# Kernel optimization log

Measured on AMD Instinct MI355X. Metric: run time of the kernel, lower is better.

Reference implementation:

```python
import jax, jax.numpy as jnp
import numpy as np

B, S, F, D, M = 2, 512, 16384, 768, 262144  # batch, seq, n_features, d_model, n_connections


def setup_inputs() -> dict:
    key = jax.random.key(0)
    k1, k2, k3, k4, k5 = jax.random.split(key, 5)
    up_facts = jax.random.normal(k1, (B, S, F), dtype=jnp.float32)
    down_encoder = jax.random.normal(k2, (F, D), dtype=jnp.float32) * 0.02
    up_decoder = jax.random.normal(k3, (D, F), dtype=jnp.float32) * 0.02
    i_indices = jnp.sort(jax.random.randint(k4, (M,), 0, F, dtype=jnp.int32)).astype(jnp.int64)
    j_indices = jax.random.randint(k5, (M,), 0, F, dtype=jnp.int32).astype(jnp.int64)
    return {
        "up_facts": up_facts,
        "down_encoder": down_encoder,
        "up_decoder": up_decoder,
        "i_indices": i_indices,
        "j_indices": j_indices,
    }


def reference(up_facts, down_encoder, up_decoder, i_indices, j_indices):
    # Virtual weight value for each sparse connection (i -> j):
    #   values[m] = <down_encoder[i_m, :], up_decoder[:, j_m]>
    values = jnp.sum(down_encoder[i_indices] * up_decoder[:, j_indices].T, axis=1)  # [M]
    # Gather upstream feature activations for each connection, scale by value.
    scaled = up_facts[:, :, j_indices] * values  # [B, S, M]
    # Scatter-add into downstream feature slots (duplicate i indices accumulate).
    contributions = jnp.zeros((up_facts.shape[0], up_facts.shape[1], down_encoder.shape[0]),
                              dtype=up_facts.dtype)
    return contributions.at[:, :, i_indices].add(scaled)  # [B, S, F]
```

## Files before the change

### kernel.cpp

```cpp
#include <hip/hip_runtime.h>
#include <hip/hip_bf16.h>

#define D_DIM 768
#define F_DIM 16384
#define M_CONN 262144
#define N_ROWS 1024

typedef float f32x4 __attribute__((ext_vector_type(4)));
typedef unsigned short u16x4 __attribute__((ext_vector_type(4)));

__device__ __forceinline__ float bf2f(unsigned short u) {
    return __uint_as_float(((unsigned int)u) << 16);
}

__global__ __launch_bounds__(512, 4) void transpose_f2b_t(const float* __restrict__ in,
                                                          unsigned short* __restrict__ out,
                                                          int R, int C) {
    __shared__ unsigned short ldsT[128][260];
    const int t = threadIdx.x;
    const int x0 = blockIdx.x * 128;
    const int y0 = blockIdx.y * 256;
    f32x4 v[16];
#pragma unroll
    for (int it = 0; it < 16; ++it) {
        const int idx = it * 512 + t;
        const int r = idx >> 5;
        const int c4 = idx & 31;
        v[it] = __builtin_nontemporal_load(
            (const f32x4*)(in + (size_t)(y0 + r) * C + x0 + c4 * 4));
    }
#pragma unroll
    for (int it = 0; it < 16; ++it) {
        const int idx = it * 512 + t;
        const int r = idx >> 5;
        const int c4 = idx & 31;
        __hip_bfloat16 b0 = __float2bfloat16(v[it].x);
        __hip_bfloat16 b1 = __float2bfloat16(v[it].y);
        __hip_bfloat16 b2 = __float2bfloat16(v[it].z);
        __hip_bfloat16 b3 = __float2bfloat16(v[it].w);
        ldsT[c4 * 4 + 0][r] = *(unsigned short*)&b0;
        ldsT[c4 * 4 + 1][r] = *(unsigned short*)&b1;
        ldsT[c4 * 4 + 2][r] = *(unsigned short*)&b2;
        ldsT[c4 * 4 + 3][r] = *(unsigned short*)&b3;
    }
    __syncthreads();
#pragma unroll
    for (int it = 0; it < 16; ++it) {
        const int idx = it * 512 + t;
        const int c = idx >> 6;
        const int r4 = idx & 63;
        const u16x4 o = *(const u16x4*)&ldsT[c][r4 * 4];
        *(u16x4*)(out + (size_t)(x0 + c) * R + y0 + r4 * 4) = o;
    }
}

__global__ __launch_bounds__(512, 4) void transpose_b2f_t(const unsigned short* __restrict__ in,
                                                          float* __restrict__ out,
                                                          int R, int C) {
    __shared__ unsigned short ldsT[256][130];
    const int t = threadIdx.x;
    const int x0 = blockIdx.x * 256;
    const int y0 = blockIdx.y * 128;
    u16x4 v[16];
#pragma unroll
    for (int it = 0; it < 16; ++it) {
        const int idx = it * 512 + t;
        const int r = idx >> 6;
        const int c4 = idx & 63;
        v[it] = __builtin_nontemporal_load(
            (const u16x4*)(in + (size_t)(y0 + r) * C + x0 + c4 * 4));
    }
#pragma unroll
    for (int it = 0; it < 16; ++it) {
        const int idx = it * 512 + t;
        const int r = idx >> 6;
        const int c4 = idx & 63;
        ldsT[c4 * 4 + 0][r] = v[it].x;
        ldsT[c4 * 4 + 1][r] = v[it].y;
        ldsT[c4 * 4 + 2][r] = v[it].z;
        ldsT[c4 * 4 + 3][r] = v[it].w;
    }
    __syncthreads();
#pragma unroll
    for (int it = 0; it < 16; ++it) {
        const int idx = it * 512 + t;
        const int c = idx >> 5;
        const int r4 = idx & 31;
        const u16x4 o = *(const u16x4*)&ldsT[c][r4 * 4];
        f32x4 f;
        f.x = bf2f(o.x); f.y = bf2f(o.y); f.z = bf2f(o.z); f.w = bf2f(o.w);
        __builtin_nontemporal_store(
            f, (f32x4*)(out + (size_t)(x0 + c) * R + y0 + r4 * 4));
    }
}

__global__ __launch_bounds__(256) void values_kernel(const float* __restrict__ de,
                                                     const unsigned short* __restrict__ udT,
                                                     const int* __restrict__ i_idx,
                                                     const int* __restrict__ j_idx,
                                                     float* __restrict__ values,
                                                     int m0) {
    const int wave = (blockIdx.x * blockDim.x + threadIdx.x) >> 6;
    const int lane = threadIdx.x & 63;
    const int mbase = m0 + wave * 4;

    int ii[4], jj[4];
#pragma unroll
    for (int t = 0; t < 4; ++t) {
        ii[t] = i_idx[mbase + t];
        jj[t] = j_idx[mbase + t];
    }
    ushort4 u[4][3];
#pragma unroll
    for (int t = 0; t < 4; ++t) {
        const ushort4* b = (const ushort4*)(udT + (size_t)jj[t] * D_DIM);
        u[t][0] = b[lane]; u[t][1] = b[lane + 64]; u[t][2] = b[lane + 128];
    }

    int cur_i = -1;
    float4 a0, a1, a2;
#pragma unroll
    for (int t = 0; t < 4; ++t) {
        const int i = ii[t];
        if (i != cur_i) {
            const float4* a = (const float4*)(de + (size_t)i * D_DIM);
            a0 = a[lane]; a1 = a[lane + 64]; a2 = a[lane + 128];
            cur_i = i;
        }
        float s = 0.f;
        s = fmaf(a0.x, bf2f(u[t][0].x), s); s = fmaf(a0.y, bf2f(u[t][0].y), s);
        s = fmaf(a0.z, bf2f(u[t][0].z), s); s = fmaf(a0.w, bf2f(u[t][0].w), s);
        s = fmaf(a1.x, bf2f(u[t][1].x), s); s = fmaf(a1.y, bf2f(u[t][1].y), s);
        s = fmaf(a1.z, bf2f(u[t][1].z), s); s = fmaf(a1.w, bf2f(u[t][1].w), s);
        s = fmaf(a2.x, bf2f(u[t][2].x), s); s = fmaf(a2.y, bf2f(u[t][2].y), s);
        s = fmaf(a2.z, bf2f(u[t][2].z), s); s = fmaf(a2.w, bf2f(u[t][2].w), s);
#pragma unroll
        for (int off = 32; off > 0; off >>= 1)
            s += __shfl_down(s, off, 64);
        if (lane == 0) values[mbase + t] = s;
    }
}

__global__ __launch_bounds__(256) void seg_kernel(const int* __restrict__ i_idx,
                                                  int* __restrict__ seg) {
    const int i = blockIdx.x * blockDim.x + threadIdx.x;
    if (i > F_DIM) return;
    if (i == F_DIM) { seg[i] = M_CONN; return; }
    int lo = 0, hi = M_CONN;
    while (lo < hi) {
        int mid = (lo + hi) >> 1;
        if (i_idx[mid] < i) lo = mid + 1; else hi = mid;
    }
    seg[i] = lo;
}

__global__ __launch_bounds__(256) void spmm_kernel(const unsigned short* __restrict__ upT,
                                                   const int* __restrict__ j_idx,
                                                   const float* __restrict__ vals,
                                                   const int* __restrict__ seg,
                                                   unsigned short* __restrict__ outT,
                                                   int i0) {
    const int i = i0 + blockIdx.x;
    const int t = threadIdx.x;
    const int ms = seg[i], me = seg[i + 1];
    float4 acc0 = make_float4(0.f, 0.f, 0.f, 0.f);
    float4 acc1 = make_float4(0.f, 0.f, 0.f, 0.f);
    float4 acc2 = make_float4(0.f, 0.f, 0.f, 0.f);
    float4 acc3 = make_float4(0.f, 0.f, 0.f, 0.f);
    int m = ms;
    for (; m + 3 < me; m += 4) {
        const int j0 = j_idx[m],     j1 = j_idx[m + 1];
        const int j2 = j_idx[m + 2], j3 = j_idx[m + 3];
        const float v0 = vals[m],     v1 = vals[m + 1];
        const float v2 = vals[m + 2], v3 = vals[m + 3];
        const ushort4 x0 = ((const ushort4*)(upT + (size_t)j0 * N_ROWS))[t];
        const ushort4 x1 = ((const ushort4*)(upT + (size_t)j1 * N_ROWS))[t];
        const ushort4 x2 = ((const ushort4*)(upT + (size_t)j2 * N_ROWS))[t];
        const ushort4 x3 = ((const ushort4*)(upT + (size_t)j3 * N_ROWS))[t];
        acc0.x = fmaf(v0, bf2f(x0.x), acc0.x); acc0.y = fmaf(v0, bf2f(x0.y), acc0.y);
        acc0.z = fmaf(v0, bf2f(x0.z), acc0.z); acc0.w = fmaf(v0, bf2f(x0.w), acc0.w);
        acc1.x = fmaf(v1, bf2f(x1.x), acc1.x); acc1.y = fmaf(v1, bf2f(x1.y), acc1.y);
        acc1.z = fmaf(v1, bf2f(x1.z), acc1.z); acc1.w = fmaf(v1, bf2f(x1.w), acc1.w);
        acc2.x = fmaf(v2, bf2f(x2.x), acc2.x); acc2.y = fmaf(v2, bf2f(x2.y), acc2.y);
        acc2.z = fmaf(v2, bf2f(x2.z), acc2.z); acc2.w = fmaf(v2, bf2f(x2.w), acc2.w);
        acc3.x = fmaf(v3, bf2f(x3.x), acc3.x); acc3.y = fmaf(v3, bf2f(x3.y), acc3.y);
        acc3.z = fmaf(v3, bf2f(x3.z), acc3.z); acc3.w = fmaf(v3, bf2f(x3.w), acc3.w);
    }
    for (; m < me; ++m) {
        const int j0 = j_idx[m];
        const float v0 = vals[m];
        const ushort4 x0 = ((const ushort4*)(upT + (size_t)j0 * N_ROWS))[t];
        acc0.x = fmaf(v0, bf2f(x0.x), acc0.x); acc0.y = fmaf(v0, bf2f(x0.y), acc0.y);
        acc0.z = fmaf(v0, bf2f(x0.z), acc0.z); acc0.w = fmaf(v0, bf2f(x0.w), acc0.w);
    }
    const float rx = (acc0.x + acc1.x) + (acc2.x + acc3.x);
    const float ry = (acc0.y + acc1.y) + (acc2.y + acc3.y);
    const float rz = (acc0.z + acc1.z) + (acc2.z + acc3.z);
    const float rw = (acc0.w + acc1.w) + (acc2.w + acc3.w);
    __hip_bfloat16 b0 = __float2bfloat16(rx);
    __hip_bfloat16 b1 = __float2bfloat16(ry);
    __hip_bfloat16 b2 = __float2bfloat16(rz);
    __hip_bfloat16 b3 = __float2bfloat16(rw);
    u16x4 o;
    o.x = *(unsigned short*)&b0;
    o.y = *(unsigned short*)&b1;
    o.z = *(unsigned short*)&b2;
    o.w = *(unsigned short*)&b3;
    __builtin_nontemporal_store(o, (u16x4*)(outT + (size_t)i * N_ROWS) + t);
}

extern "C" void kernel_launch(void* const* d_in, const int* in_sizes, int n_in,
                              void* d_out, int out_size, void* d_ws, size_t ws_size,
                              hipStream_t stream) {
    const float* up_facts = (const float*)d_in[0];
    const float* de       = (const float*)d_in[1];
    const float* ud       = (const float*)d_in[2];
    const int*   i_idx    = (const int*)d_in[3];
    const int*   j_idx    = (const int*)d_in[4];
    float* out = (float*)d_out;

    char* ws = (char*)d_ws;
    unsigned short* udT  = (unsigned short*)ws;
    unsigned short* outT = (unsigned short*)(ws + (size_t)24 * 1024 * 1024);
    float* values = (float*)(ws + (size_t)64 * 1024 * 1024);
    int*   seg    = (int*)  (ws + (size_t)65 * 1024 * 1024);
    unsigned short* upT = (unsigned short*)out;

    transpose_f2b_t<<<dim3(F_DIM / 128, D_DIM / 256), 512, 0, stream>>>(
        ud, udT, D_DIM, F_DIM);
    for (int h = 0; h < 2; ++h)
        values_kernel<<<(M_CONN / 8) * 64 / 256, 256, 0, stream>>>(
            de, udT, i_idx, j_idx, values, h * (M_CONN / 2));
    transpose_f2b_t<<<dim3(F_DIM / 128, N_ROWS / 256), 512, 0, stream>>>(
        up_facts, upT, N_ROWS, F_DIM);
    seg_kernel<<<(F_DIM + 1 + 255) / 256, 256, 0, stream>>>(i_idx, seg);
    for (int q = 0; q < 4; ++q)
        spmm_kernel<<<F_DIM / 4, 256, 0, stream>>>(upT, j_idx, values, seg, outT,
                                                   q * (F_DIM / 4));
    transpose_b2f_t<<<dim3(N_ROWS / 256, F_DIM / 128), 512, 0, stream>>>(
        outT, out, F_DIM, N_ROWS);
}
```

Baseline: 341.2 us.

## Fuse transposes, fold segment build into values kernel, merge split launches

Merges the two fp32-to-bf16 transposes into one launch that picks its source by blockIdx.y. Folds the segment-offset computation into the values kernel: each wave's lane 0 fills seg entries by scanning boundaries in the sorted i indices, replacing the separate binary-search kernel. The split loops of values and spmm launches become single full-size launches. The goal is fewer kernel launches and serialization gaps, at the cost of a serial per-wave segment fill with a long loop for large index gaps.

```diff
diff --git a/kernel.cpp b/kernel.cpp
--- a/kernel.cpp
+++ b/kernel.cpp
@@ -13,13 +13,20 @@
     return __uint_as_float(((unsigned int)u) << 16);
 }
 
-__global__ __launch_bounds__(512, 4) void transpose_f2b_t(const float* __restrict__ in,
-                                                          unsigned short* __restrict__ out,
-                                                          int R, int C) {
+__global__ __launch_bounds__(512, 4) void transpose_f2b_fused(
+        const float* __restrict__ inA, unsigned short* __restrict__ outA, int RA, int yA,
+        const float* __restrict__ inB, unsigned short* __restrict__ outB, int RB) {
+    const int C = F_DIM;
+    const float* in;
+    unsigned short* out;
+    int R, yb;
+    if (blockIdx.y < (unsigned)yA) { in = inA; out = outA; R = RA; yb = blockIdx.y; }
+    else                           { in = inB; out = outB; R = RB; yb = blockIdx.y - yA; }
+
     __shared__ unsigned short ldsT[128][260];
     const int t = threadIdx.x;
     const int x0 = blockIdx.x * 128;
-    const int y0 = blockIdx.y * 256;
+    const int y0 = yb * 256;
     f32x4 v[16];
 #pragma unroll
     for (int it = 0; it < 16; ++it) {
@@ -99,10 +106,10 @@
                                                      const int* __restrict__ i_idx,
                                                      const int* __restrict__ j_idx,
                                                      float* __restrict__ values,
-                                                     int m0) {
+                                                     int* __restrict__ seg) {
     const int wave = (blockIdx.x * blockDim.x + threadIdx.x) >> 6;
     const int lane = threadIdx.x & 63;
-    const int mbase = m0 + wave * 4;
+    const int mbase = wave * 4;
 
     int ii[4], jj[4];
 #pragma unroll
@@ -110,6 +117,19 @@
         ii[t] = i_idx[mbase + t];
         jj[t] = j_idx[mbase + t];
     }
+
+    if (lane == 0) {
+        int prev = (mbase == 0) ? -1 : i_idx[mbase - 1];
+#pragma unroll
+        for (int t = 0; t < 4; ++t) {
+            const int cur = ii[t];
+            for (int k = prev + 1; k <= cur; ++k) seg[k] = mbase + t;
+            prev = cur;
+        }
+        if (mbase + 4 == M_CONN)
+            for (int k = prev + 1; k <= F_DIM; ++k) seg[k] = M_CONN;
+    }
+
     ushort4 u[4][3];
 #pragma unroll
     for (int t = 0; t < 4; ++t) {
@@ -141,26 +161,12 @@
     }
 }
 
-__global__ __launch_bounds__(256) void seg_kernel(const int* __restrict__ i_idx,
-                                                  int* __restrict__ seg) {
-    const int i = blockIdx.x * blockDim.x + threadIdx.x;
-    if (i > F_DIM) return;
-    if (i == F_DIM) { seg[i] = M_CONN; return; }
-    int lo = 0, hi = M_CONN;
-    while (lo < hi) {
-        int mid = (lo + hi) >> 1;
-        if (i_idx[mid] < i) lo = mid + 1; else hi = mid;
-    }
-    seg[i] = lo;
-}
-
 __global__ __launch_bounds__(256) void spmm_kernel(const unsigned short* __restrict__ upT,
                                                    const int* __restrict__ j_idx,
                                                    const float* __restrict__ vals,
                                                    const int* __restrict__ seg,
-                                                   unsigned short* __restrict__ outT,
-                                                   int i0) {
-    const int i = i0 + blockIdx.x;
+                                                   unsigned short* __restrict__ outT) {
+    const int i = blockIdx.x;
     const int t = threadIdx.x;
     const int ms = seg[i], me = seg[i + 1];
     float4 acc0 = make_float4(0.f, 0.f, 0.f, 0.f);
@@ -226,17 +232,11 @@
     int*   seg    = (int*)  (ws + (size_t)65 * 1024 * 1024);
     unsigned short* upT = (unsigned short*)out;
 
-    transpose_f2b_t<<<dim3(F_DIM / 128, D_DIM / 256), 512, 0, stream>>>(
-        ud, udT, D_DIM, F_DIM);
-    for (int h = 0; h < 2; ++h)
-        values_kernel<<<(M_CONN / 8) * 64 / 256, 256, 0, stream>>>(
-            de, udT, i_idx, j_idx, values, h * (M_CONN / 2));
-    transpose_f2b_t<<<dim3(F_DIM / 128, N_ROWS / 256), 512, 0, stream>>>(
-        up_facts, upT, N_ROWS, F_DIM);
-    seg_kernel<<<(F_DIM + 1 + 255) / 256, 256, 0, stream>>>(i_idx, seg);
-    for (int q = 0; q < 4; ++q)
-        spmm_kernel<<<F_DIM / 4, 256, 0, stream>>>(upT, j_idx, values, seg, outT,
-                                                   q * (F_DIM / 4));
+    transpose_f2b_fused<<<dim3(F_DIM / 128, D_DIM / 256 + N_ROWS / 256), 512, 0, stream>>>(
+        ud, udT, D_DIM, D_DIM / 256, up_facts, upT, N_ROWS);
+    values_kernel<<<(M_CONN / 4) * 64 / 256, 256, 0, stream>>>(
+        de, udT, i_idx, j_idx, values, seg);
+    spmm_kernel<<<F_DIM, 256, 0, stream>>>(upT, j_idx, values, seg, outT);
     transpose_b2f_t<<<dim3(N_ROWS / 256, F_DIM / 128), 512, 0, stream>>>(
         outT, out, F_DIM, N_ROWS);
 }
```

After: 323.7 us. -5.1%, faster.
